# Performance work log

Measured on AMD Instinct MI355X. Metric: run time of the kernel, lower is better.

## Reference

```python
import jax, jax.numpy as jnp
import numpy as np

D = 1024
DFF = 4096  # SwiGLU hidden = 4*d_model
EPS = 1e-6

def rmsnorm(x, w):
    return x * jax.lax.rsqrt(jnp.mean(x * x, axis=-1, keepdims=True) + EPS) * w

def mingru_scan(gates, cands):
    # h_t = g_t * h_{t-1} + (1 - g_t) * c_t, h_0 = 0 -> linear recurrence,
    # solved with an associative scan over pairs (a, b): h = a*h_prev + b.
    a = gates
    b = (1.0 - gates) * cands
    def combine(e1, e2):
        a1, b1 = e1
        a2, b2 = e2
        return (a1 * a2, a2 * b1 + b2)
    _, h = jax.lax.associative_scan(combine, (a, b), axis=1)
    return h

def setup_inputs() -> dict:
    key = jax.random.key(0)
    ks = jax.random.split(key, 10)
    xavier = lambda k, fan_in, fan_out: jax.random.uniform(
        k, (fan_in, fan_out), jnp.float32,
        -np.sqrt(6.0 / (fan_in + fan_out)), np.sqrt(6.0 / (fan_in + fan_out)))
    return {
        "x": jax.random.normal(ks[0], (4, 4096, D), jnp.float32),
        "Wg": xavier(ks[1], D, D),
        "bg": jnp.ones((D,), jnp.float32),   # gate bias init = 1.0
        "Wc": xavier(ks[2], D, D),
        "bc": jnp.zeros((D,), jnp.float32),
        "n1_w": jnp.ones((D,), jnp.float32),
        "n2_w": jnp.ones((D,), jnp.float32),
        "W1": xavier(ks[3], D, DFF),   # SwiGLU gate proj
        "W3": xavier(ks[4], D, DFF),   # SwiGLU up proj
        "W2": xavier(ks[5], DFF, D),   # SwiGLU down proj
    }

def reference(x, Wg, bg, Wc, bc, n1_w, n2_w, W1, W3, W2):
    # --- MinGRU sub-block (pre-norm, residual) ---
    h_in = rmsnorm(x, n1_w)
    gates = jax.nn.sigmoid(jnp.einsum('bld,de->ble', h_in, Wg) + bg)
    cands = jnp.tanh(jnp.einsum('bld,de->ble', h_in, Wc) + bc)
    x = x + mingru_scan(gates, cands)
    # --- SwiGLU FFN sub-block (pre-norm, residual) ---
    f_in = rmsnorm(x, n2_w)
    ff = jnp.einsum('blf,fd->bld',
                    jax.nn.silu(jnp.einsum('bld,df->blf', f_in, W1))
                    * jnp.einsum('bld,df->blf', f_in, W3), W2)
    return x + ff
```

## Files before the change

kernel.cpp:

```cpp
#include <hip/hip_runtime.h>
#include <hip/hip_bf16.h>
#include <math.h>

typedef __bf16 bf16_t;
typedef bf16_t bf16x8 __attribute__((ext_vector_type(8)));
typedef bf16_t bf16x4 __attribute__((ext_vector_type(4)));
typedef float f32x4 __attribute__((ext_vector_type(4)));

#define D_MODEL 1024
#define SEQ     4096
#define BATCH   4
#define NTOK    16384
#define DFF     4096
#define CLEN    64
#define NCHUNK  64
#define NCH     4096

__global__ void transpose_to_bf16(const float* __restrict__ W,
                                  bf16_t* __restrict__ Wt, int R, int C) {
    __shared__ float tile[32][33];
    const int c0 = blockIdx.x * 32, r0 = blockIdx.y * 32;
    const int tx = threadIdx.x, ty = threadIdx.y;
#pragma unroll
    for (int j = 0; j < 32; j += 8)
        tile[ty + j][tx] = W[(size_t)(r0 + ty + j) * C + c0 + tx];
    __syncthreads();
#pragma unroll
    for (int j = 0; j < 32; j += 8)
        Wt[(size_t)(c0 + ty + j) * R + r0 + tx] = (bf16_t)tile[tx][ty + j];
}

__global__ void rmsnorm_kernel(const float* __restrict__ x,
                               const float* __restrict__ w,
                               bf16_t* __restrict__ out) {
    const int row = blockIdx.x;
    const int tid = threadIdx.x;
    const float4 v = ((const float4*)(x + (size_t)row * D_MODEL))[tid];
    float ss = v.x * v.x + v.y * v.y + v.z * v.z + v.w * v.w;
#pragma unroll
    for (int o = 1; o < 64; o <<= 1) ss += __shfl_xor(ss, o);
    __shared__ float red[4];
    if ((tid & 63) == 0) red[tid >> 6] = ss;
    __syncthreads();
    const float tot = red[0] + red[1] + red[2] + red[3];
    const float scale = rsqrtf(tot * (1.0f / D_MODEL) + 1e-6f);
    const float4 wv = ((const float4*)w)[tid];
    bf16x4 o4;
    o4[0] = (bf16_t)(v.x * scale * wv.x);
    o4[1] = (bf16_t)(v.y * scale * wv.y);
    o4[2] = (bf16_t)(v.z * scale * wv.z);
    o4[3] = (bf16_t)(v.w * scale * wv.w);
    ((bf16x4*)(out + (size_t)row * D_MODEL))[tid] = o4;
}

template <int MODE>
__global__ __launch_bounds__(256, 2)
void gemm_dual(const bf16_t* __restrict__ A, const bf16_t* __restrict__ B1t,
               const bf16_t* __restrict__ B2t, const float* __restrict__ bias1,
               const float* __restrict__ bias2, float* __restrict__ O1,
               float* __restrict__ O2, bf16_t* __restrict__ Ot, int N, int K) {
    __shared__ bf16_t As[128][40];
    __shared__ bf16_t B1s[128][40];
    __shared__ bf16_t B2s[128][40];
    const int tid = threadIdx.x;
    const int bn = blockIdx.x, bm = blockIdx.y;
    const int sRow = tid >> 1, sCol = (tid & 1) << 4;
    const bf16_t* Ag  = A   + (size_t)(bm * 128 + sRow) * K + sCol;
    const bf16_t* B1g = B1t + (size_t)(bn * 128 + sRow) * K + sCol;
    const bf16_t* B2g = B2t + (size_t)(bn * 128 + sRow) * K + sCol;
    const int lane = tid & 63;
    const int wr = (tid >> 7) & 1, wc = (tid >> 6) & 1;
    const int lr = lane & 15, lk = lane >> 4;

    f32x4 acc1[4][4] = {};
    f32x4 acc2[4][4] = {};
    for (int k0 = 0; k0 < K; k0 += 32) {
        bf16x8 a0  = *(const bf16x8*)(Ag + k0);
        bf16x8 a1  = *(const bf16x8*)(Ag + k0 + 8);
        bf16x8 b10 = *(const bf16x8*)(B1g + k0);
        bf16x8 b11 = *(const bf16x8*)(B1g + k0 + 8);
        bf16x8 b20 = *(const bf16x8*)(B2g + k0);
        bf16x8 b21 = *(const bf16x8*)(B2g + k0 + 8);
        __syncthreads();
        *(bf16x8*)&As[sRow][sCol]      = a0;
        *(bf16x8*)&As[sRow][sCol + 8]  = a1;
        *(bf16x8*)&B1s[sRow][sCol]     = b10;
        *(bf16x8*)&B1s[sRow][sCol + 8] = b11;
        *(bf16x8*)&B2s[sRow][sCol]     = b20;
        *(bf16x8*)&B2s[sRow][sCol + 8] = b21;
        __syncthreads();
        bf16x8 af[4], b1f[4], b2f[4];
#pragma unroll
        for (int m = 0; m < 4; ++m)
            af[m] = *(const bf16x8*)&As[wr * 64 + m * 16 + lr][lk * 8];
#pragma unroll
        for (int n = 0; n < 4; ++n) {
            b1f[n] = *(const bf16x8*)&B1s[wc * 64 + n * 16 + lr][lk * 8];
            b2f[n] = *(const bf16x8*)&B2s[wc * 64 + n * 16 + lr][lk * 8];
        }
#pragma unroll
        for (int m = 0; m < 4; ++m)
#pragma unroll
            for (int n = 0; n < 4; ++n) {
                acc1[m][n] = __builtin_amdgcn_mfma_f32_16x16x32_bf16(
                    af[m], b1f[n], acc1[m][n], 0, 0, 0);
                acc2[m][n] = __builtin_amdgcn_mfma_f32_16x16x32_bf16(
                    af[m], b2f[n], acc2[m][n], 0, 0, 0);
            }
    }
    const int rowBase = bm * 128 + wr * 64;
    const int colBase = bn * 128 + wc * 64;
#pragma unroll
    for (int n = 0; n < 4; ++n) {
        const int col = colBase + n * 16 + lr;
        float b1v = 0.f, b2v = 0.f;
        if (MODE == 0) { b1v = bias1[col]; b2v = bias2[col]; }
#pragma unroll
        for (int m = 0; m < 4; ++m) {
#pragma unroll
            for (int j = 0; j < 4; ++j) {
                const int row = rowBase + m * 16 + lk * 4 + j;
                const size_t idx = (size_t)row * N + col;
                if (MODE == 0) {
                    const float gv = 1.0f / (1.0f + __expf(-(acc1[m][n][j] + b1v)));
                    const float cv = tanhf(acc2[m][n][j] + b2v);
                    O1[idx] = gv;
                    O2[idx] = cv;
                } else {
                    const float a = acc1[m][n][j];
                    const float s = a / (1.0f + __expf(-a));
                    Ot[idx] = (bf16_t)(s * acc2[m][n][j]);
                }
            }
        }
    }
}

__global__ __launch_bounds__(256, 2)
void gemm_res(const bf16_t* __restrict__ A, const bf16_t* __restrict__ Bt,
              float* O, int N, int K) {
    __shared__ bf16_t As[128][40];
    __shared__ bf16_t Bs[128][40];
    const int tid = threadIdx.x;
    const int bn = blockIdx.x, bm = blockIdx.y;
    const int sRow = tid >> 1, sCol = (tid & 1) << 4;
    const bf16_t* Ag = A  + (size_t)(bm * 128 + sRow) * K + sCol;
    const bf16_t* Bg = Bt + (size_t)(bn * 128 + sRow) * K + sCol;
    const int lane = tid & 63;
    const int wr = (tid >> 7) & 1, wc = (tid >> 6) & 1;
    const int lr = lane & 15, lk = lane >> 4;

    f32x4 acc[4][4] = {};
    for (int k0 = 0; k0 < K; k0 += 32) {
        bf16x8 a0 = *(const bf16x8*)(Ag + k0);
        bf16x8 a1 = *(const bf16x8*)(Ag + k0 + 8);
        bf16x8 b0 = *(const bf16x8*)(Bg + k0);
        bf16x8 b1 = *(const bf16x8*)(Bg + k0 + 8);
        __syncthreads();
        *(bf16x8*)&As[sRow][sCol]     = a0;
        *(bf16x8*)&As[sRow][sCol + 8] = a1;
        *(bf16x8*)&Bs[sRow][sCol]     = b0;
        *(bf16x8*)&Bs[sRow][sCol + 8] = b1;
        __syncthreads();
        bf16x8 af[4], bf[4];
#pragma unroll
        for (int m = 0; m < 4; ++m)
            af[m] = *(const bf16x8*)&As[wr * 64 + m * 16 + lr][lk * 8];
#pragma unroll
        for (int n = 0; n < 4; ++n)
            bf[n] = *(const bf16x8*)&Bs[wc * 64 + n * 16 + lr][lk * 8];
#pragma unroll
        for (int m = 0; m < 4; ++m)
#pragma unroll
            for (int n = 0; n < 4; ++n)
                acc[m][n] = __builtin_amdgcn_mfma_f32_16x16x32_bf16(
                    af[m], bf[n], acc[m][n], 0, 0, 0);
    }
    const int rowBase = bm * 128 + wr * 64;
    const int colBase = bn * 128 + wc * 64;
#pragma unroll
    for (int n = 0; n < 4; ++n) {
        const int col = colBase + n * 16 + lr;
#pragma unroll
        for (int m = 0; m < 4; ++m) {
#pragma unroll
            for (int j = 0; j < 4; ++j) {
                const int row = rowBase + m * 16 + lk * 4 + j;
                const size_t idx = (size_t)row * N + col;
                O[idx] += acc[m][n][j];
            }
        }
    }
}

__global__ void scan_phase1(const float* __restrict__ g,
                            const float* __restrict__ c,
                            float* __restrict__ cA, float* __restrict__ cB) {
    const int d = blockIdx.x * 256 + threadIdx.x;
    const int b = blockIdx.y;
    const int cidx = blockIdx.z;
    const int ch = b * D_MODEL + d;
    const size_t base = ((size_t)b * SEQ + (size_t)cidx * CLEN) * D_MODEL + d;
    float A = 1.0f, Bv = 0.0f;
#pragma unroll 4
    for (int t = 0; t < CLEN; ++t) {
        const float gv = g[base + (size_t)t * D_MODEL];
        const float cv = c[base + (size_t)t * D_MODEL];
        Bv = gv * Bv + (1.0f - gv) * cv;
        A *= gv;
    }
    cA[cidx * NCH + ch] = A;
    cB[cidx * NCH + ch] = Bv;
}

__global__ void scan_phase2(const float* __restrict__ cA,
                            const float* __restrict__ cB,
                            float* __restrict__ hstart) {
    const int ch = blockIdx.x * 256 + threadIdx.x;
    float h = 0.0f;
    for (int cdx = 0; cdx < NCHUNK; ++cdx) {
        hstart[cdx * NCH + ch] = h;
        h = cA[cdx * NCH + ch] * h + cB[cdx * NCH + ch];
    }
}

__global__ void scan_phase3(const float* __restrict__ g,
                            const float* __restrict__ c,
                            const float* __restrict__ hstart,
                            const float* __restrict__ x,
                            float* __restrict__ x1) {
    const int d = blockIdx.x * 256 + threadIdx.x;
    const int b = blockIdx.y;
    const int cidx = blockIdx.z;
    const int ch = b * D_MODEL + d;
    const size_t base = ((size_t)b * SEQ + (size_t)cidx * CLEN) * D_MODEL + d;
    float h = hstart[cidx * NCH + ch];
#pragma unroll 4
    for (int t = 0; t < CLEN; ++t) {
        const size_t off = base + (size_t)t * D_MODEL;
        const float gv = g[off];
        const float cv = c[off];
        h = gv * h + (1.0f - gv) * cv;
        x1[off] = x[off] + h;
    }
}

extern "C" void kernel_launch(void* const* d_in, const int* in_sizes, int n_in,
                              void* d_out, int out_size, void* d_ws,
                              size_t ws_size, hipStream_t stream) {
    const float* x   = (const float*)d_in[0];
    const float* Wg  = (const float*)d_in[1];
    const float* bg  = (const float*)d_in[2];
    const float* Wc  = (const float*)d_in[3];
    const float* bc  = (const float*)d_in[4];
    const float* n1w = (const float*)d_in[5];
    const float* n2w = (const float*)d_in[6];
    const float* W1  = (const float*)d_in[7];
    const float* W3  = (const float*)d_in[8];
    const float* W2  = (const float*)d_in[9];
    float* out = (float*)d_out;

    char* p = (char*)d_ws;
    bf16_t* h_in = (bf16_t*)p;  p += (size_t)NTOK * D_MODEL * 2;
    bf16_t* f_in = (bf16_t*)p;  p += (size_t)NTOK * D_MODEL * 2;
    bf16_t* Wg_t = (bf16_t*)p;  p += (size_t)D_MODEL * D_MODEL * 2;
    bf16_t* Wc_t = (bf16_t*)p;  p += (size_t)D_MODEL * D_MODEL * 2;
    bf16_t* W1_t = (bf16_t*)p;  p += (size_t)DFF * D_MODEL * 2;
    bf16_t* W3_t = (bf16_t*)p;  p += (size_t)DFF * D_MODEL * 2;
    bf16_t* W2_t = (bf16_t*)p;  p += (size_t)D_MODEL * DFF * 2;
    float* cA     = (float*)p;  p += (size_t)NCHUNK * NCH * 4;
    float* cB     = (float*)p;  p += (size_t)NCHUNK * NCH * 4;
    float* hstart = (float*)p;  p += (size_t)NCHUNK * NCH * 4;
    float* gbuf   = (float*)p;  p += (size_t)NTOK * D_MODEL * 4;
    float* cbuf   = (float*)p;  p += (size_t)NTOK * D_MODEL * 4;
    bf16_t* tbuf  = (bf16_t*)gbuf;

    const dim3 tb(32, 8);
    transpose_to_bf16<<<dim3(1024 / 32, 1024 / 32), tb, 0, stream>>>(Wg, Wg_t, 1024, 1024);
    transpose_to_bf16<<<dim3(1024 / 32, 1024 / 32), tb, 0, stream>>>(Wc, Wc_t, 1024, 1024);
    transpose_to_bf16<<<dim3(4096 / 32, 1024 / 32), tb, 0, stream>>>(W1, W1_t, 1024, 4096);
    transpose_to_bf16<<<dim3(4096 / 32, 1024 / 32), tb, 0, stream>>>(W3, W3_t, 1024, 4096);
    transpose_to_bf16<<<dim3(1024 / 32, 4096 / 32), tb, 0, stream>>>(W2, W2_t, 4096, 1024);

    rmsnorm_kernel<<<NTOK, 256, 0, stream>>>(x, n1w, h_in);

    gemm_dual<0><<<dim3(D_MODEL / 128, NTOK / 128), 256, 0, stream>>>(
        h_in, Wg_t, Wc_t, bg, bc, gbuf, cbuf, nullptr, D_MODEL, D_MODEL);

    scan_phase1<<<dim3(D_MODEL / 256, BATCH, NCHUNK), 256, 0, stream>>>(gbuf, cbuf, cA, cB);
    scan_phase2<<<NCH / 256, 256, 0, stream>>>(cA, cB, hstart);
    scan_phase3<<<dim3(D_MODEL / 256, BATCH, NCHUNK), 256, 0, stream>>>(gbuf, cbuf, hstart, x, out);

    rmsnorm_kernel<<<NTOK, 256, 0, stream>>>(out, n2w, f_in);

    gemm_dual<1><<<dim3(DFF / 128, NTOK / 128), 256, 0, stream>>>(
        f_in, W1_t, W3_t, nullptr, nullptr, nullptr, nullptr, tbuf, DFF, D_MODEL);

    gemm_res<<<dim3(D_MODEL / 128, NTOK / 128), 256, 0, stream>>>(tbuf, W2_t, out, D_MODEL, DFF);
}
```

Baseline: 900.4 us.

## Use direct global-to-LDS loads in GEMMs and pack gate/candidate as bf16 pairs

Result: faster. 847.9 us (-5.8%).

```diff
diff --git a/kernel.cpp b/kernel.cpp
--- a/kernel.cpp
+++ b/kernel.cpp
@@ -5,6 +5,7 @@
 typedef __bf16 bf16_t;
 typedef bf16_t bf16x8 __attribute__((ext_vector_type(8)));
 typedef bf16_t bf16x4 __attribute__((ext_vector_type(4)));
+typedef bf16_t bf16x2 __attribute__((ext_vector_type(2)));
 typedef float f32x4 __attribute__((ext_vector_type(4)));
 
 #define D_MODEL 1024
@@ -15,6 +16,12 @@
 #define CLEN    64
 #define NCHUNK  64
 #define NCH     4096
+
+__device__ __forceinline__ void gload16(const bf16_t* g, bf16_t* l) {
+    __builtin_amdgcn_global_load_lds(
+        (const __attribute__((address_space(1))) void*)g,
+        (__attribute__((address_space(3))) void*)l, 16, 0, 0);
+}
 
 __global__ void transpose_to_bf16(const float* __restrict__ W,
                                   bf16_t* __restrict__ Wt, int R, int C) {
@@ -57,46 +64,51 @@
 __global__ __launch_bounds__(256, 2)
 void gemm_dual(const bf16_t* __restrict__ A, const bf16_t* __restrict__ B1t,
                const bf16_t* __restrict__ B2t, const float* __restrict__ bias1,
-               const float* __restrict__ bias2, float* __restrict__ O1,
-               float* __restrict__ O2, bf16_t* __restrict__ Ot, int N, int K) {
-    __shared__ bf16_t As[128][40];
-    __shared__ bf16_t B1s[128][40];
-    __shared__ bf16_t B2s[128][40];
+               const float* __restrict__ bias2, bf16x2* __restrict__ GC,
+               bf16_t* __restrict__ Ot, int N, int K) {
+    __shared__ bf16_t As[128 * 32];
+    __shared__ bf16_t B1s[128 * 32];
+    __shared__ bf16_t B2s[128 * 32];
     const int tid = threadIdx.x;
+    const int lane = tid & 63;
+    const int wave = tid >> 6;
     const int bn = blockIdx.x, bm = blockIdx.y;
-    const int sRow = tid >> 1, sCol = (tid & 1) << 4;
-    const bf16_t* Ag  = A   + (size_t)(bm * 128 + sRow) * K + sCol;
-    const bf16_t* B1g = B1t + (size_t)(bn * 128 + sRow) * K + sCol;
-    const bf16_t* B2g = B2t + (size_t)(bn * 128 + sRow) * K + sCol;
-    const int lane = tid & 63;
-    const int wr = (tid >> 7) & 1, wc = (tid >> 6) & 1;
+
+    const int stR = wave * 16 + (lane >> 2);
+    const int stC = (lane & 3) * 8;
+    const bf16_t* Ag  = A   + (size_t)(bm * 128 + stR) * K + stC;
+    const bf16_t* B1g = B1t + (size_t)(bn * 128 + stR) * K + stC;
+    const bf16_t* B2g = B2t + (size_t)(bn * 128 + stR) * K + stC;
+    bf16_t* Al0  = &As [(wave * 16) * 32];
+    bf16_t* Al1  = &As [(64 + wave * 16) * 32];
+    bf16_t* B1l0 = &B1s[(wave * 16) * 32];
+    bf16_t* B1l1 = &B1s[(64 + wave * 16) * 32];
+    bf16_t* B2l0 = &B2s[(wave * 16) * 32];
+    bf16_t* B2l1 = &B2s[(64 + wave * 16) * 32];
+    const size_t row64 = (size_t)64 * K;
+
+    const int wr = wave >> 1, wc = wave & 1;
     const int lr = lane & 15, lk = lane >> 4;
 
     f32x4 acc1[4][4] = {};
     f32x4 acc2[4][4] = {};
     for (int k0 = 0; k0 < K; k0 += 32) {
-        bf16x8 a0  = *(const bf16x8*)(Ag + k0);
-        bf16x8 a1  = *(const bf16x8*)(Ag + k0 + 8);
-        bf16x8 b10 = *(const bf16x8*)(B1g + k0);
-        bf16x8 b11 = *(const bf16x8*)(B1g + k0 + 8);
-        bf16x8 b20 = *(const bf16x8*)(B2g + k0);
-        bf16x8 b21 = *(const bf16x8*)(B2g + k0 + 8);
         __syncthreads();
-        *(bf16x8*)&As[sRow][sCol]      = a0;
-        *(bf16x8*)&As[sRow][sCol + 8]  = a1;
-        *(bf16x8*)&B1s[sRow][sCol]     = b10;
-        *(bf16x8*)&B1s[sRow][sCol + 8] = b11;
-        *(bf16x8*)&B2s[sRow][sCol]     = b20;
-        *(bf16x8*)&B2s[sRow][sCol + 8] = b21;
+        gload16(Ag  + k0,         Al0);
+        gload16(Ag  + k0 + row64, Al1);
+        gload16(B1g + k0,         B1l0);
+        gload16(B1g + k0 + row64, B1l1);
+        gload16(B2g + k0,         B2l0);
+        gload16(B2g + k0 + row64, B2l1);
         __syncthreads();
         bf16x8 af[4], b1f[4], b2f[4];
 #pragma unroll
         for (int m = 0; m < 4; ++m)
-            af[m] = *(const bf16x8*)&As[wr * 64 + m * 16 + lr][lk * 8];
+            af[m] = *(const bf16x8*)&As[(wr * 64 + m * 16 + lr) * 32 + lk * 8];
 #pragma unroll
         for (int n = 0; n < 4; ++n) {
-            b1f[n] = *(const bf16x8*)&B1s[wc * 64 + n * 16 + lr][lk * 8];
-            b2f[n] = *(const bf16x8*)&B2s[wc * 64 + n * 16 + lr][lk * 8];
+            b1f[n] = *(const bf16x8*)&B1s[(wc * 64 + n * 16 + lr) * 32 + lk * 8];
+            b2f[n] = *(const bf16x8*)&B2s[(wc * 64 + n * 16 + lr) * 32 + lk * 8];
         }
 #pragma unroll
         for (int m = 0; m < 4; ++m)
@@ -124,8 +136,10 @@
                 if (MODE == 0) {
                     const float gv = 1.0f / (1.0f + __expf(-(acc1[m][n][j] + b1v)));
                     const float cv = tanhf(acc2[m][n][j] + b2v);
-                    O1[idx] = gv;
-                    O2[idx] = cv;
+                    bf16x2 pk;
+                    pk[0] = (bf16_t)gv;
+                    pk[1] = (bf16_t)cv;
+                    GC[idx] = pk;
                 } else {
                     const float a = acc1[m][n][j];
                     const float s = a / (1.0f + __expf(-a));
@@ -139,36 +153,41 @@
 __global__ __launch_bounds__(256, 2)
 void gemm_res(const bf16_t* __restrict__ A, const bf16_t* __restrict__ Bt,
               float* O, int N, int K) {
-    __shared__ bf16_t As[128][40];
-    __shared__ bf16_t Bs[128][40];
+    __shared__ bf16_t As[128 * 32];
+    __shared__ bf16_t Bs[128 * 32];
     const int tid = threadIdx.x;
+    const int lane = tid & 63;
+    const int wave = tid >> 6;
     const int bn = blockIdx.x, bm = blockIdx.y;
-    const int sRow = tid >> 1, sCol = (tid & 1) << 4;
-    const bf16_t* Ag = A  + (size_t)(bm * 128 + sRow) * K + sCol;
-    const bf16_t* Bg = Bt + (size_t)(bn * 128 + sRow) * K + sCol;
-    const int lane = tid & 63;
-    const int wr = (tid >> 7) & 1, wc = (tid >> 6) & 1;
+
+    const int stR = wave * 16 + (lane >> 2);
+    const int stC = (lane & 3) * 8;
+    const bf16_t* Ag = A  + (size_t)(bm * 128 + stR) * K + stC;
+    const bf16_t* Bg = Bt + (size_t)(bn * 128 + stR) * K + stC;
+    bf16_t* Al0 = &As[(wave * 16) * 32];
+    bf16_t* Al1 = &As[(64 + wave * 16) * 32];
+    bf16_t* Bl0 = &Bs[(wave * 16) * 32];
+    bf16_t* Bl1 = &Bs[(64 + wave * 16) * 32];
+    const size_t row64 = (size_t)64 * K;
+
+    const int wr = wave >> 1, wc = wave & 1;
     const int lr = lane & 15, lk = lane >> 4;
 
     f32x4 acc[4][4] = {};
     for (int k0 = 0; k0 < K; k0 += 32) {
-        bf16x8 a0 = *(const bf16x8*)(Ag + k0);
-        bf16x8 a1 = *(const bf16x8*)(Ag + k0 + 8);
-        bf16x8 b0 = *(const bf16x8*)(Bg + k0);
-        bf16x8 b1 = *(const bf16x8*)(Bg + k0 + 8);
         __syncthreads();
-        *(bf16x8*)&As[sRow][sCol]     = a0;
-        *(bf16x8*)&As[sRow][sCol + 8] = a1;
-        *(bf16x8*)&Bs[sRow][sCol]     = b0;
-        *(bf16x8*)&Bs[sRow][sCol + 8] = b1;
+        gload16(Ag + k0,         Al0);
+        gload16(Ag + k0 + row64, Al1);
+        gload16(Bg + k0,         Bl0);
+        gload16(Bg + k0 + row64, Bl1);
         __syncthreads();
         bf16x8 af[4], bf[4];
 #pragma unroll
         for (int m = 0; m < 4; ++m)
-            af[m] = *(const bf16x8*)&As[wr * 64 + m * 16 + lr][lk * 8];
+            af[m] = *(const bf16x8*)&As[(wr * 64 + m * 16 + lr) * 32 + lk * 8];
 #pragma unroll
         for (int n = 0; n < 4; ++n)
-            bf[n] = *(const bf16x8*)&Bs[wc * 64 + n * 16 + lr][lk * 8];
+            bf[n] = *(const bf16x8*)&Bs[(wc * 64 + n * 16 + lr) * 32 + lk * 8];
 #pragma unroll
         for (int m = 0; m < 4; ++m)
 #pragma unroll
@@ -193,8 +212,7 @@
     }
 }
 
-__global__ void scan_phase1(const float* __restrict__ g,
-                            const float* __restrict__ c,
+__global__ void scan_phase1(const bf16x2* __restrict__ gc,
                             float* __restrict__ cA, float* __restrict__ cB) {
     const int d = blockIdx.x * 256 + threadIdx.x;
     const int b = blockIdx.y;
@@ -202,10 +220,10 @@
     const int ch = b * D_MODEL + d;
     const size_t base = ((size_t)b * SEQ + (size_t)cidx * CLEN) * D_MODEL + d;
     float A = 1.0f, Bv = 0.0f;
-#pragma unroll 4
+#pragma unroll 8
     for (int t = 0; t < CLEN; ++t) {
-        const float gv = g[base + (size_t)t * D_MODEL];
-        const float cv = c[base + (size_t)t * D_MODEL];
+        const bf16x2 v = gc[base + (size_t)t * D_MODEL];
+        const float gv = (float)v[0], cv = (float)v[1];
         Bv = gv * Bv + (1.0f - gv) * cv;
         A *= gv;
     }
@@ -218,14 +236,14 @@
                             float* __restrict__ hstart) {
     const int ch = blockIdx.x * 256 + threadIdx.x;
     float h = 0.0f;
+#pragma unroll 8
     for (int cdx = 0; cdx < NCHUNK; ++cdx) {
         hstart[cdx * NCH + ch] = h;
         h = cA[cdx * NCH + ch] * h + cB[cdx * NCH + ch];
     }
 }
 
-__global__ void scan_phase3(const float* __restrict__ g,
-                            const float* __restrict__ c,
+__global__ void scan_phase3(const bf16x2* __restrict__ gc,
                             const float* __restrict__ hstart,
                             const float* __restrict__ x,
                             float* __restrict__ x1) {
@@ -235,11 +253,11 @@
     const int ch = b * D_MODEL + d;
     const size_t base = ((size_t)b * SEQ + (size_t)cidx * CLEN) * D_MODEL + d;
     float h = hstart[cidx * NCH + ch];
-#pragma unroll 4
+#pragma unroll 8
     for (int t = 0; t < CLEN; ++t) {
         const size_t off = base + (size_t)t * D_MODEL;
-        const float gv = g[off];
-        const float cv = c[off];
+        const bf16x2 v = gc[off];
+        const float gv = (float)v[0], cv = (float)v[1];
         h = gv * h + (1.0f - gv) * cv;
         x1[off] = x[off] + h;
     }
@@ -261,19 +279,19 @@
     float* out = (float*)d_out;
 
     char* p = (char*)d_ws;
-    bf16_t* h_in = (bf16_t*)p;  p += (size_t)NTOK * D_MODEL * 2;
-    bf16_t* f_in = (bf16_t*)p;  p += (size_t)NTOK * D_MODEL * 2;
-    bf16_t* Wg_t = (bf16_t*)p;  p += (size_t)D_MODEL * D_MODEL * 2;
-    bf16_t* Wc_t = (bf16_t*)p;  p += (size_t)D_MODEL * D_MODEL * 2;
-    bf16_t* W1_t = (bf16_t*)p;  p += (size_t)DFF * D_MODEL * 2;
-    bf16_t* W3_t = (bf16_t*)p;  p += (size_t)DFF * D_MODEL * 2;
-    bf16_t* W2_t = (bf16_t*)p;  p += (size_t)D_MODEL * DFF * 2;
-    float* cA     = (float*)p;  p += (size_t)NCHUNK * NCH * 4;
-    float* cB     = (float*)p;  p += (size_t)NCHUNK * NCH * 4;
-    float* hstart = (float*)p;  p += (size_t)NCHUNK * NCH * 4;
-    float* gbuf   = (float*)p;  p += (size_t)NTOK * D_MODEL * 4;
-    float* cbuf   = (float*)p;  p += (size_t)NTOK * D_MODEL * 4;
-    bf16_t* tbuf  = (bf16_t*)gbuf;
+    bf16_t* tbuf  = (bf16_t*)p;
+    bf16_t* h_in  = (bf16_t*)p;  p += (size_t)NTOK * D_MODEL * 2;
+    bf16x2* gcbuf = (bf16x2*)p;  p += (size_t)NTOK * D_MODEL * 4;
+    p += (size_t)32 << 20;
+    bf16_t* f_in  = (bf16_t*)p;  p += (size_t)NTOK * D_MODEL * 2;
+    bf16_t* Wg_t  = (bf16_t*)p;  p += (size_t)D_MODEL * D_MODEL * 2;
+    bf16_t* Wc_t  = (bf16_t*)p;  p += (size_t)D_MODEL * D_MODEL * 2;
+    bf16_t* W1_t  = (bf16_t*)p;  p += (size_t)DFF * D_MODEL * 2;
+    bf16_t* W3_t  = (bf16_t*)p;  p += (size_t)DFF * D_MODEL * 2;
+    bf16_t* W2_t  = (bf16_t*)p;  p += (size_t)D_MODEL * DFF * 2;
+    float* cA     = (float*)p;   p += (size_t)NCHUNK * NCH * 4;
+    float* cB     = (float*)p;   p += (size_t)NCHUNK * NCH * 4;
+    float* hstart = (float*)p;   p += (size_t)NCHUNK * NCH * 4;
 
     const dim3 tb(32, 8);
     transpose_to_bf16<<<dim3(1024 / 32, 1024 / 32), tb, 0, stream>>>(Wg, Wg_t, 1024, 1024);
@@ -285,16 +303,16 @@
     rmsnorm_kernel<<<NTOK, 256, 0, stream>>>(x, n1w, h_in);
 
     gemm_dual<0><<<dim3(D_MODEL / 128, NTOK / 128), 256, 0, stream>>>(
-        h_in, Wg_t, Wc_t, bg, bc, gbuf, cbuf, nullptr, D_MODEL, D_MODEL);
-
-    scan_phase1<<<dim3(D_MODEL / 256, BATCH, NCHUNK), 256, 0, stream>>>(gbuf, cbuf, cA, cB);
+        h_in, Wg_t, Wc_t, bg, bc, gcbuf, nullptr, D_MODEL, D_MODEL);
+
+    scan_phase1<<<dim3(D_MODEL / 256, BATCH, NCHUNK), 256, 0, stream>>>(gcbuf, cA, cB);
     scan_phase2<<<NCH / 256, 256, 0, stream>>>(cA, cB, hstart);
-    scan_phase3<<<dim3(D_MODEL / 256, BATCH, NCHUNK), 256, 0, stream>>>(gbuf, cbuf, hstart, x, out);
+    scan_phase3<<<dim3(D_MODEL / 256, BATCH, NCHUNK), 256, 0, stream>>>(gcbuf, hstart, x, out);
 
     rmsnorm_kernel<<<NTOK, 256, 0, stream>>>(out, n2w, f_in);
 
     gemm_dual<1><<<dim3(DFF / 128, NTOK / 128), 256, 0, stream>>>(
-        f_in, W1_t, W3_t, nullptr, nullptr, nullptr, nullptr, tbuf, DFF, D_MODEL);
+        f_in, W1_t, W3_t, nullptr, nullptr, nullptr, tbuf, DFF, D_MODEL);
 
     gemm_res<<<dim3(D_MODEL / 128, NTOK / 128), 256, 0, stream>>>(tbuf, W2_t, out, D_MODEL, DFF);
 }
```
